# Kernel tuning notes

Measured on AMD Instinct MI355X. Metric: run time of the kernel, lower is better.

The kernel has to match this reference:

```python
import jax, jax.numpy as jnp
import numpy as np

B, T, C = 8, 1024, 1024   # batch, seq (== block_size), n_embed
H, D = 16, 64             # num_heads, head_size


def setup_inputs() -> dict:
    key = jax.random.key(0)
    kx, kq, kk, kv = jax.random.split(key, 4)
    scale = C ** -0.5  # mimic nn.Linear init scale roughly
    return {
        "x": jax.random.normal(kx, (B, T, C), dtype=jnp.float32),
        "Wq": jax.random.normal(kq, (H, C, D), dtype=jnp.float32) * scale,
        "Wk": jax.random.normal(kk, (H, C, D), dtype=jnp.float32) * scale,
        "Wv": jax.random.normal(kv, (H, C, D), dtype=jnp.float32) * scale,
    }


def reference(x, Wq, Wk, Wv):
    # Per-head Q/K/V projections (batched over heads instead of a Python loop)
    q = jnp.einsum("btc,hcd->bhtd", x, Wq)
    k = jnp.einsum("btc,hcd->bhtd", x, Wk)
    v = jnp.einsum("btc,hcd->bhtd", x, Wv)

    # scaled causal attention scores: [B, H, T, T]
    scores = jnp.einsum("bhtd,bhsd->bhts", q, k) * (D ** -0.5)
    causal = jnp.tril(jnp.ones((T, T), dtype=bool))
    scores = jnp.where(causal, scores, jnp.finfo(scores.dtype).min)
    attn = jax.nn.softmax(scores, axis=-1)

    out = jnp.einsum("bhts,bhsd->bhtd", attn, v)  # [B, H, T, D]
    # concat heads along last dim -> [B, T, H*D]
    return out.transpose(0, 2, 1, 3).reshape(B, T, H * D)
```

## Files before the change

kernel.cpp:

```cpp
#include <hip/hip_runtime.h>
#include <hip/hip_bf16.h>
#include <cstdint>


typedef __attribute__((ext_vector_type(8))) short short8;
typedef __attribute__((ext_vector_type(4))) short bfs4;
typedef __attribute__((ext_vector_type(4))) float f32x4;
typedef __attribute__((ext_vector_type(4))) int   i32x4;

typedef const __attribute__((address_space(1))) void* gas1_t;
typedef __attribute__((address_space(3))) void* las3_t;

__device__ __forceinline__ void gl_lds16(const void* g, void* l) {
  __builtin_amdgcn_global_load_lds((gas1_t)g, (las3_t)l, 16, 0, 0);
}

__device__ __forceinline__ unsigned short f2bf(float f) {
  union { float f; unsigned int u; } v; v.f = f;
  unsigned int u = v.u;
  return (unsigned short)((u + 0x7fffu + ((u >> 16) & 1u)) >> 16);
}

__device__ __forceinline__ unsigned int pk_bf16(float a, float b) {
  union { __hip_bfloat162 h; unsigned int u; } cv;
  cv.h = __float22bfloat162_rn(make_float2(a, b));
  return cv.u;
}

__global__ __launch_bounds__(256) void k_convert_x(const float* __restrict__ x,
                                                   unsigned short* __restrict__ xb) {
  int g = blockIdx.x * 256 + threadIdx.x;
  const float4* xp = (const float4*)x + (size_t)g * 2;
  float4 a = xp[0], b = xp[1];
  short8 o;
  o[0] = (short)f2bf(a.x); o[1] = (short)f2bf(a.y);
  o[2] = (short)f2bf(a.z); o[3] = (short)f2bf(a.w);
  o[4] = (short)f2bf(b.x); o[5] = (short)f2bf(b.y);
  o[6] = (short)f2bf(b.z); o[7] = (short)f2bf(b.w);
  *(short8*)(xb + (size_t)g * 8) = o;
}

__global__ __launch_bounds__(256) void k_convert_w(const float* __restrict__ Wq,
                                                   const float* __restrict__ Wk,
                                                   const float* __restrict__ Wv,
                                                   unsigned short* __restrict__ Wt) {
  int g = blockIdx.x * 256 + threadIdx.x;
  int d  = g & 63;
  int cb = (g >> 6) & 127;
  int h  = (g >> 13) & 15;
  int p  = g >> 17;
  const float* W = (p == 0) ? Wq : (p == 1) ? Wk : Wv;
  const float* src = W + ((size_t)h * 1024 + cb * 8) * 64 + d;
  short8 o;
#pragma unroll
  for (int j = 0; j < 8; ++j) o[j] = (short)f2bf(src[(size_t)j * 64]);
  *(short8*)(Wt + (((size_t)p * 16 + h) * 64 + d) * 1024 + cb * 8) = o;
}

__global__ __launch_bounds__(256) void k_proj(const unsigned short* __restrict__ xb,
                                              const unsigned short* __restrict__ Wt,
                                              unsigned short* __restrict__ Qb,
                                              unsigned short* __restrict__ Kb,
                                              unsigned short* __restrict__ Vt) {
  __shared__ alignas(16) unsigned short As[8192];
  __shared__ alignas(16) unsigned short Bs[8192];
  const int p   = blockIdx.y;
  const int bx  = blockIdx.x;
  const int tid = threadIdx.x;
  const int lane = tid & 63, w = tid >> 6;
  const int ln = lane & 15, quad = lane >> 4;
  const int wm = w >> 1, wn = w & 1;

  const unsigned short* Abase;
  const unsigned short* Bbase;
  int m0, n0;
  const int c = bx & 7, j = bx >> 3;
  if (p < 2) {
    Abase = xb; Bbase = Wt + (size_t)p * 1048576;
    m0 = ((j >> 3) * 8 + c) * 128;
    n0 = (j & 7) * 128;
  } else {
    Abase = Wt + (size_t)2 * 1048576; Bbase = xb;
    n0 = ((j >> 3) * 8 + c) * 128;
    m0 = (j & 7) * 128;
  }

  i32x4 ra[4], rb[4];
  auto ld = [&](int kt) {
    const int c0 = kt * 64;
#pragma unroll
    for (int i = 0; i < 4; ++i) {
      int idx = i * 256 + tid;
      int iln = idx & 15, iq = (idx >> 4) & 3, imt = (idx >> 6) & 7, ikk = (idx >> 9) & 1;
      int row = imt * 16 + iln;
      int col = c0 + ikk * 32 + iq * 8;
      ra[i] = *(const i32x4*)(Abase + (size_t)(m0 + row) * 1024 + col);
      rb[i] = *(const i32x4*)(Bbase + (size_t)(n0 + row) * 1024 + col);
    }
  };

  f32x4 acc[4][4];
#pragma unroll
  for (int i = 0; i < 4; ++i)
#pragma unroll
    for (int jj = 0; jj < 4; ++jj) acc[i][jj] = (f32x4){0.f, 0.f, 0.f, 0.f};

  ld(0);
  for (int kt = 0; kt < 16; ++kt) {
#pragma unroll
    for (int i = 0; i < 4; ++i) {
      *(i32x4*)((char*)As + (size_t)(i * 256 + tid) * 16) = ra[i];
      *(i32x4*)((char*)Bs + (size_t)(i * 256 + tid) * 16) = rb[i];
    }
    __syncthreads();
    if (kt < 15) ld(kt + 1);

#pragma unroll
    for (int kk = 0; kk < 2; ++kk) {
      short8 af[4], bfr[4];
#pragma unroll
      for (int t4 = 0; t4 < 4; ++t4) {
        af[t4]  = *(const short8*)&As[(size_t)((((kk * 8 + wm * 4 + t4) * 4 + quad) * 16 + ln)) * 8];
        bfr[t4] = *(const short8*)&Bs[(size_t)((((kk * 8 + wn * 4 + t4) * 4 + quad) * 16 + ln)) * 8];
      }
#pragma unroll
      for (int mt = 0; mt < 4; ++mt)
#pragma unroll
        for (int nt = 0; nt < 4; ++nt)
          acc[mt][nt] = __builtin_amdgcn_mfma_f32_16x16x32_bf16(
              af[mt], bfr[nt], acc[mt][nt], 0, 0, 0);
    }
    __syncthreads();
  }

  unsigned short* outp = (p == 0) ? Qb : (p == 1) ? Kb : Vt;
#pragma unroll
  for (int mt = 0; mt < 4; ++mt)
#pragma unroll
    for (int nt = 0; nt < 4; ++nt)
#pragma unroll
      for (int r = 0; r < 4; ++r) {
        int m = m0 + (wm * 4 + mt) * 16 + quad * 4 + r;
        int n = n0 + (wn * 4 + nt) * 16 + ln;
        size_t addr;
        if (p < 2) {
          addr = ((size_t)(m >> 10) * 16 + (n >> 6)) * 65536 + (size_t)(m & 1023) * 64 + (n & 63);
        } else {
          addr = ((size_t)(n >> 10) * 1024 + m) * 1024 + (n & 1023);
        }
        outp[addr] = f2bf(acc[mt][nt][r]);
      }
}

__global__ __launch_bounds__(256) void k_attn(const unsigned short* __restrict__ Qb,
                                              const unsigned short* __restrict__ Kb,
                                              const unsigned short* __restrict__ Vt,
                                              float* __restrict__ out) {
  __shared__ alignas(16) unsigned short Ks[4096];
  __shared__ alignas(16) unsigned short Vs[4096];
  __shared__ alignas(16) unsigned short Ps[4096];
  const int bid = blockIdx.x;
  const int qb = 15 - (bid >> 7);
  const int bh = bid & 127;
  const int b = bh >> 4, h = bh & 15;
  const int tid = threadIdx.x, lane = tid & 63, w = tid >> 6;
  const int ln = lane & 15, quad = lane >> 4;
  const int q = qb * 64 + w * 16 + ln;

  short8 qf[2];
#pragma unroll
  for (int kk = 0; kk < 2; ++kk)
    qf[kk] = *(const short8*)(Qb + ((size_t)bh * 1024 + q) * 64 + kk * 32 + quad * 8);

  f32x4 o[4];
#pragma unroll
  for (int dt = 0; dt < 4; ++dt) o[dt] = (f32x4){0.f, 0.f, 0.f, 0.f};
  float l_i = 0.f;
  const float sc = 0.18033688011112042f;
  const float FM = 16.0f;

  for (int kt = 0; kt <= qb; ++kt) {
    const int s0 = kt * 64;
    __syncthreads();
#pragma unroll
    for (int i = 0; i < 2; ++i) {
      int idx = i * 256 + tid;
      int iln = idx & 15, iq = (idx >> 4) & 3, ikk = (idx >> 6) & 1, it = (idx >> 7) & 3;
      char* lk = (char*)Ks + (size_t)(i * 256 + (tid & ~63)) * 16;
      char* lv = (char*)Vs + (size_t)(i * 256 + (tid & ~63)) * 16;
      gl_lds16(Kb + ((size_t)bh * 1024 + s0 + it * 16 + iln) * 64 + ikk * 32 + iq * 8, lk);
      gl_lds16(Vt + ((size_t)bh * 64 + it * 16 + iln) * 1024 + s0 + ikk * 32 + iq * 8, lv);
    }
    __builtin_amdgcn_s_waitcnt(0);
    __syncthreads();

    f32x4 st[4];
#pragma unroll
    for (int s = 0; s < 4; ++s) {
      st[s] = (f32x4){0.f, 0.f, 0.f, 0.f};
#pragma unroll
      for (int kk = 0; kk < 2; ++kk) {
        short8 kf = *(const short8*)&Ks[(size_t)(((s * 2 + kk) * 4 + quad) * 16 + ln) * 8];
        st[s] = __builtin_amdgcn_mfma_f32_16x16x32_bf16(kf, qf[kk], st[s], 0, 0, 0);
      }
    }

    const bool diag = (kt == qb);
    float pv[4][4];
    float rs = 0.f;
#pragma unroll
    for (int s = 0; s < 4; ++s)
#pragma unroll
      for (int r = 0; r < 4; ++r) {
        float v = fmaf(st[s][r], sc, -FM);
        if (diag) {
          int sidx = s0 + s * 16 + quad * 4 + r;
          if (sidx > q) v = -1.0e30f;
        }
        float e = __builtin_amdgcn_exp2f(v);
        pv[s][r] = e;
        rs += e;
      }
    rs += __shfl_xor(rs, 16);
    rs += __shfl_xor(rs, 32);
    l_i += rs;

    unsigned short* Pq = Ps + w * 1024;
#pragma unroll
    for (int s = 0; s < 4; ++s) {
      union { bfs4 v; unsigned int u[2]; } pk;
      pk.u[0] = pk_bf16(pv[s][0], pv[s][1]);
      pk.u[1] = pk_bf16(pv[s][2], pv[s][3]);
      *(bfs4*)&Pq[(s * 2 + (quad >> 1)) * 128 + ln * 8 + (quad & 1) * 4] = pk.v;
    }

#pragma unroll
    for (int kk = 0; kk < 2; ++kk) {
      short8 pf = *(const short8*)&Pq[(size_t)((kk * 4 + quad) * 16 + ln) * 8];
#pragma unroll
      for (int dt = 0; dt < 4; ++dt) {
        short8 vf = *(const short8*)&Vs[(size_t)(((dt * 2 + kk) * 4 + quad) * 16 + ln) * 8];
        o[dt] = __builtin_amdgcn_mfma_f32_16x16x32_bf16(vf, pf, o[dt], 0, 0, 0);
      }
    }
  }

  const float rl = 1.0f / l_i;
#pragma unroll
  for (int dt = 0; dt < 4; ++dt) {
    float4 ov;
    ov.x = o[dt][0] * rl; ov.y = o[dt][1] * rl;
    ov.z = o[dt][2] * rl; ov.w = o[dt][3] * rl;
    *(float4*)(out + ((size_t)b * 1024 + q) * 1024 + h * 64 + dt * 16 + quad * 4) = ov;
  }
}

extern "C" void kernel_launch(void* const* d_in, const int* in_sizes, int n_in,
                              void* d_out, int out_size, void* d_ws, size_t ws_size,
                              hipStream_t stream) {
  const float* x  = (const float*)d_in[0];
  const float* Wq = (const float*)d_in[1];
  const float* Wk = (const float*)d_in[2];
  const float* Wv = (const float*)d_in[3];
  float* out = (float*)d_out;

  unsigned short* ws = (unsigned short*)d_ws;
  unsigned short* xb = ws;
  unsigned short* Wt = ws + 8388608;
  unsigned short* Qb = ws + 11534336;
  unsigned short* Kb = ws + 19922944;
  unsigned short* Vt = ws + 28311552;

  hipLaunchKernelGGL(k_convert_x, dim3(4096), dim3(256), 0, stream, x, xb);
  hipLaunchKernelGGL(k_convert_w, dim3(1536), dim3(256), 0, stream, Wq, Wk, Wv, Wt);
  hipLaunchKernelGGL(k_proj, dim3(512, 3), dim3(256), 0, stream, xb, Wt, Qb, Kb, Vt);
  hipLaunchKernelGGL(k_attn, dim3(2048), dim3(256), 0, stream, Qb, Kb, Vt, out);
}
```

Measured before the change: 233.0 us.

## Use single-wave attention blocks loading K/V directly into registers

The attention kernel shrinks from four-wave blocks sharing K/V tiles in LDS to one-wave blocks of 16 queries. Each wave loads its K and V fragments straight from global memory into registers, which removes the global-to-LDS copies and both __syncthreads per tile. The trade-off is that K/V reuse across the four query sub-tiles is lost, so global/L2 traffic for K and V roughly quadruples. The grid grows to 8192 smaller blocks, and the causal loop is now bounded per 16-query tile.

Result: slower. 318.6 us (+36.8%).

```diff
diff --git a/kernel.cpp b/kernel.cpp
--- a/kernel.cpp
+++ b/kernel.cpp
@@ -7,13 +7,6 @@
 typedef __attribute__((ext_vector_type(4))) short bfs4;
 typedef __attribute__((ext_vector_type(4))) float f32x4;
 typedef __attribute__((ext_vector_type(4))) int   i32x4;
-
-typedef const __attribute__((address_space(1))) void* gas1_t;
-typedef __attribute__((address_space(3))) void* las3_t;
-
-__device__ __forceinline__ void gl_lds16(const void* g, void* l) {
-  __builtin_amdgcn_global_load_lds((gas1_t)g, (las3_t)l, 16, 0, 0);
-}
 
 __device__ __forceinline__ unsigned short f2bf(float f) {
   union { float f; unsigned int u; } v; v.f = f;
@@ -152,25 +145,26 @@
       }
 }
 
-__global__ __launch_bounds__(256) void k_attn(const unsigned short* __restrict__ Qb,
-                                              const unsigned short* __restrict__ Kb,
-                                              const unsigned short* __restrict__ Vt,
-                                              float* __restrict__ out) {
-  __shared__ alignas(16) unsigned short Ks[4096];
-  __shared__ alignas(16) unsigned short Vs[4096];
-  __shared__ alignas(16) unsigned short Ps[4096];
+__global__ __launch_bounds__(64) void k_attn(const unsigned short* __restrict__ Qb,
+                                             const unsigned short* __restrict__ Kb,
+                                             const unsigned short* __restrict__ Vt,
+                                             float* __restrict__ out) {
+  __shared__ alignas(16) unsigned short Ps[1024];
   const int bid = blockIdx.x;
-  const int qb = 15 - (bid >> 7);
+  const int qt16 = 63 - (bid >> 7);
   const int bh = bid & 127;
   const int b = bh >> 4, h = bh & 15;
-  const int tid = threadIdx.x, lane = tid & 63, w = tid >> 6;
+  const int lane = threadIdx.x & 63;
   const int ln = lane & 15, quad = lane >> 4;
-  const int q = qb * 64 + w * 16 + ln;
+  const int q = qt16 * 16 + ln;
 
   short8 qf[2];
 #pragma unroll
   for (int kk = 0; kk < 2; ++kk)
     qf[kk] = *(const short8*)(Qb + ((size_t)bh * 1024 + q) * 64 + kk * 32 + quad * 8);
+
+  const unsigned short* Kp = Kb + ((size_t)bh * 1024 + ln) * 64 + quad * 8;
+  const unsigned short* Vp = Vt + ((size_t)bh * 64 + ln) * 1024 + quad * 8;
 
   f32x4 o[4];
 #pragma unroll
@@ -179,37 +173,38 @@
   const float sc = 0.18033688011112042f;
   const float FM = 16.0f;
 
-  for (int kt = 0; kt <= qb; ++kt) {
+  const int ktmax = qt16 >> 2;
+  for (int kt = 0; kt <= ktmax; ++kt) {
     const int s0 = kt * 64;
-    __syncthreads();
-#pragma unroll
-    for (int i = 0; i < 2; ++i) {
-      int idx = i * 256 + tid;
-      int iln = idx & 15, iq = (idx >> 4) & 3, ikk = (idx >> 6) & 1, it = (idx >> 7) & 3;
-      char* lk = (char*)Ks + (size_t)(i * 256 + (tid & ~63)) * 16;
-      char* lv = (char*)Vs + (size_t)(i * 256 + (tid & ~63)) * 16;
-      gl_lds16(Kb + ((size_t)bh * 1024 + s0 + it * 16 + iln) * 64 + ikk * 32 + iq * 8, lk);
-      gl_lds16(Vt + ((size_t)bh * 64 + it * 16 + iln) * 1024 + s0 + ikk * 32 + iq * 8, lv);
-    }
-    __builtin_amdgcn_s_waitcnt(0);
-    __syncthreads();
+
+    short8 kf[8];
+#pragma unroll
+    for (int s = 0; s < 4; ++s)
+#pragma unroll
+      for (int kk = 0; kk < 2; ++kk)
+        kf[s * 2 + kk] = *(const short8*)(Kp + (size_t)(s0 + s * 16) * 64 + kk * 32);
+
+    short8 vf[8];
+#pragma unroll
+    for (int dt = 0; dt < 4; ++dt)
+#pragma unroll
+      for (int kk = 0; kk < 2; ++kk)
+        vf[dt * 2 + kk] = *(const short8*)(Vp + (size_t)dt * 16384 + s0 + kk * 32);
 
     f32x4 st[4];
 #pragma unroll
     for (int s = 0; s < 4; ++s) {
       st[s] = (f32x4){0.f, 0.f, 0.f, 0.f};
 #pragma unroll
-      for (int kk = 0; kk < 2; ++kk) {
-        short8 kf = *(const short8*)&Ks[(size_t)(((s * 2 + kk) * 4 + quad) * 16 + ln) * 8];
-        st[s] = __builtin_amdgcn_mfma_f32_16x16x32_bf16(kf, qf[kk], st[s], 0, 0, 0);
-      }
-    }
-
-    const bool diag = (kt == qb);
-    float pv[4][4];
+      for (int kk = 0; kk < 2; ++kk)
+        st[s] = __builtin_amdgcn_mfma_f32_16x16x32_bf16(kf[s * 2 + kk], qf[kk], st[s], 0, 0, 0);
+    }
+
+    const bool diag = (kt == ktmax);
     float rs = 0.f;
 #pragma unroll
-    for (int s = 0; s < 4; ++s)
+    for (int s = 0; s < 4; ++s) {
+      float e[4];
 #pragma unroll
       for (int r = 0; r < 4; ++r) {
         float v = fmaf(st[s][r], sc, -FM);
@@ -217,31 +212,24 @@
           int sidx = s0 + s * 16 + quad * 4 + r;
           if (sidx > q) v = -1.0e30f;
         }
-        float e = __builtin_amdgcn_exp2f(v);
-        pv[s][r] = e;
-        rs += e;
+        e[r] = __builtin_amdgcn_exp2f(v);
+        rs += e[r];
       }
+      union { bfs4 v; unsigned int u[2]; } pk;
+      pk.u[0] = pk_bf16(e[0], e[1]);
+      pk.u[1] = pk_bf16(e[2], e[3]);
+      *(bfs4*)&Ps[(s * 2 + (quad >> 1)) * 128 + ln * 8 + (quad & 1) * 4] = pk.v;
+    }
     rs += __shfl_xor(rs, 16);
     rs += __shfl_xor(rs, 32);
     l_i += rs;
 
-    unsigned short* Pq = Ps + w * 1024;
-#pragma unroll
-    for (int s = 0; s < 4; ++s) {
-      union { bfs4 v; unsigned int u[2]; } pk;
-      pk.u[0] = pk_bf16(pv[s][0], pv[s][1]);
-      pk.u[1] = pk_bf16(pv[s][2], pv[s][3]);
-      *(bfs4*)&Pq[(s * 2 + (quad >> 1)) * 128 + ln * 8 + (quad & 1) * 4] = pk.v;
-    }
-
-#pragma unroll
-    for (int kk = 0; kk < 2; ++kk) {
-      short8 pf = *(const short8*)&Pq[(size_t)((kk * 4 + quad) * 16 + ln) * 8];
-#pragma unroll
-      for (int dt = 0; dt < 4; ++dt) {
-        short8 vf = *(const short8*)&Vs[(size_t)(((dt * 2 + kk) * 4 + quad) * 16 + ln) * 8];
-        o[dt] = __builtin_amdgcn_mfma_f32_16x16x32_bf16(vf, pf, o[dt], 0, 0, 0);
-      }
+#pragma unroll
+    for (int kkl = 0; kkl < 2; ++kkl) {
+      short8 pf = *(const short8*)&Ps[(size_t)((kkl * 4 + quad) * 16 + ln) * 8];
+#pragma unroll
+      for (int dt = 0; dt < 4; ++dt)
+        o[dt] = __builtin_amdgcn_mfma_f32_16x16x32_bf16(vf[dt * 2 + kkl], pf, o[dt], 0, 0, 0);
     }
   }
 
@@ -274,5 +262,5 @@
   hipLaunchKernelGGL(k_convert_x, dim3(4096), dim3(256), 0, stream, x, xb);
   hipLaunchKernelGGL(k_convert_w, dim3(1536), dim3(256), 0, stream, Wq, Wk, Wv, Wt);
   hipLaunchKernelGGL(k_proj, dim3(512, 3), dim3(256), 0, stream, xb, Wt, Qb, Kb, Vt);
-  hipLaunchKernelGGL(k_attn, dim3(2048), dim3(256), 0, stream, Qb, Kb, Vt, out);
-}
+  hipLaunchKernelGGL(k_attn, dim3(8192), dim3(64), 0, stream, Qb, Kb, Vt, out);
+}
```
